# Kernel tuning notes

Measured on AMD Instinct MI355X. Metric: run time of the kernel, lower is better.

The kernel has to match this reference:

```python
import jax, jax.numpy as jnp
from jax import lax
import numpy as np

DN = ('NCH', 'OIH', 'NCH')

def conv1d(x, w, b, stride, pad):
    # x: (B,C,L), w: (O,I,K) torch Conv1d layout
    y = lax.conv_general_dilated(x, w, (stride,), [(pad, pad)], dimension_numbers=DN)
    return y + b[None, :, None]

def convt1d(x, w, b, stride, pad, out_pad):
    # w: (I,O,K) torch ConvTranspose1d layout -> flip + swap to (O,I,K)
    k = w.shape[-1]
    w2 = jnp.flip(w, -1).transpose(1, 0, 2)
    y = lax.conv_general_dilated(x, w2, (1,), [(k - 1 - pad, k - 1 - pad + out_pad)],
                                 lhs_dilation=(stride,), dimension_numbers=DN)
    return y + b[None, :, None]

def setup_inputs() -> dict:
    key = jax.random.key(0)
    ks = iter(jax.random.split(key, 32))
    def w_init(k, shape):
        fan_in = shape[1] * shape[2]
        return jax.random.normal(k, shape, jnp.float32) * (1.0 / np.sqrt(fan_in))
    inp = {}
    inp['waveform'] = jax.random.normal(next(ks), (8, 65536), jnp.float32)
    # encoder Conv1d weights (O,I,K)
    enc_shapes = [(64, 1, 15), (128, 64, 15), (256, 128, 15), (512, 256, 15), (512, 512, 7)]
    for i, s in enumerate(enc_shapes, 1):
        inp[f'e{i}w'] = w_init(next(ks), s)
        inp[f'e{i}b'] = jnp.zeros((s[0],), jnp.float32)
    # codebook, uniform(-1/K, 1/K) as in torch init
    K = 1024
    inp['codebook'] = jax.random.uniform(next(ks), (K, 512), jnp.float32, -1.0 / K, 1.0 / K)
    # decoder ConvTranspose1d weights (I,O,K)
    dec_shapes = [(512, 512, 7), (512, 256, 15), (256, 128, 15), (128, 64, 15), (64, 1, 15)]
    for i, s in enumerate(dec_shapes, 1):
        inp[f'd{i}w'] = w_init(next(ks), (s[1], s[0], s[2])).transpose(1, 0, 2)
        inp[f'd{i}b'] = jnp.zeros((s[1],), jnp.float32)
    return inp

def reference(waveform, e1w, e1b, e2w, e2b, e3w, e3b, e4w, e4b, e5w, e5b,
              codebook, d1w, d1b, d2w, d2b, d3w, d3b, d4w, d4b, d5w, d5b):
    elu = jax.nn.elu
    x = waveform[:, None, :]                       # (B,1,T)
    x = elu(conv1d(x, e1w, e1b, 1, 7))
    x = elu(conv1d(x, e2w, e2b, 2, 7))
    x = elu(conv1d(x, e3w, e3b, 2, 7))
    x = elu(conv1d(x, e4w, e4b, 2, 7))
    x = conv1d(x, e5w, e5b, 1, 3)                  # (B,D,T')
    emb = x.transpose(0, 2, 1)                     # (B,T',D)
    B, Tq, D = emb.shape
    flat = emb.reshape(-1, D)                      # (N,D)
    dists = (jnp.sum(flat * flat, axis=1, keepdims=True)
             + jnp.sum(codebook * codebook, axis=1)
             - 2.0 * flat @ codebook.T)            # (N,K)
    idx = jnp.argmin(dists, axis=1)                # (N,)
    q_flat = codebook[idx]                         # gather == one-hot matmul
    quantized = q_flat.reshape(B, Tq, D)
    commitment_loss = 0.25 * jnp.mean((lax.stop_gradient(quantized) - emb) ** 2)
    quantized_st = emb + lax.stop_gradient(quantized - emb)
    codes = idx.reshape(B, Tq)
    y = quantized_st.transpose(0, 2, 1)            # (B,D,T')
    y = elu(convt1d(y, d1w, d1b, 1, 3, 0))
    y = elu(convt1d(y, d2w, d2b, 2, 7, 1))
    y = elu(convt1d(y, d3w, d3b, 2, 7, 1))
    y = elu(convt1d(y, d4w, d4b, 2, 7, 1))
    y = jnp.tanh(convt1d(y, d5w, d5b, 1, 7, 0))    # (B,1,T)
    reconstructed = y[:, 0, :]                     # (B,T)
    recon_loss = jnp.mean(jnp.abs(reconstructed - waveform))
    return reconstructed, quantized_st, codes, commitment_loss, recon_loss
```

## Files before the change

kernel.cpp:

```cpp
#include <hip/hip_runtime.h>
#include <hip/hip_bf16.h>
#include <math.h>

#define DEV __device__ __forceinline__

typedef __attribute__((ext_vector_type(8))) short s16x8;
typedef __attribute__((ext_vector_type(4))) float f32x4;

DEV float elu_f(float v) { return v > 0.0f ? v : (float)expm1((double)v); }
DEV float elu_fast(float v) { return v > 0.0f ? v : expm1f(v); }

DEV unsigned short f2bf(float f) {
  unsigned u = __float_as_uint(f);
  return (unsigned short)((u + 0x7fffu + ((u >> 16) & 1u)) >> 16);
}
DEV float bf2f(unsigned short s) { return __uint_as_float(((unsigned)s) << 16); }

constexpr int ceil_div_c(int a, int b) { return (a > 0) ? (a + b - 1) / b : -((-a) / b); }

template<int K, int S, int PAD, int ACT>
__global__ __launch_bounds__(256) void conv1d_k(
    const float* __restrict__ x, const float* __restrict__ w,
    const float* __restrict__ bias, float* __restrict__ y,
    int Cin, int Cout, int Lin, int Lout)
{
  constexpr int PT = 8;
  constexpr int W  = (PT - 1) * S + K;
  constexpr int M0 = (4 - (PAD & 3)) & 3;
  constexpr int NQ = (M0 + W + 3) / 4;
  constexpr int CC = 16;
  constexpr int KP = (K + 3) & ~3;

  const int lane = threadIdx.x & 63;
  const int wv   = threadIdx.x >> 6;
  const int b    = blockIdx.z;
  const int cob  = blockIdx.y * 16;
  const int t0   = (blockIdx.x * 64 + lane) * PT;

  __shared__ __align__(16) float wl[16][CC][KP];

  float acc[4][PT];
  #pragma unroll
  for (int cc = 0; cc < 4; ++cc)
    #pragma unroll
    for (int g = 0; g < PT; ++g) acc[cc][g] = 0.0f;

  const float* xb  = x + (size_t)b * Cin * Lin;
  const int start = t0 * S - PAD;
  const int vbase = start - M0;
  const bool fast = (vbase >= 0) && (vbase + 4 * NQ <= Lin);

  for (int c0 = 0; c0 < Cin; c0 += CC) {
    const int cn = (Cin - c0 < CC) ? (Cin - c0) : CC;
    __syncthreads();
    for (int i = threadIdx.x; i < 16 * cn * K; i += 256) {
      int cc  = i / (cn * K);
      int rem = i - cc * (cn * K);
      int ci  = rem / K;
      int k   = rem - ci * K;
      wl[cc][ci][k] = w[((size_t)(cob + cc) * Cin + (c0 + ci)) * K + k];
    }
    __syncthreads();
    #pragma unroll 1
    for (int ci = 0; ci < cn; ++ci) {
      const float* xp = xb + (size_t)(c0 + ci) * Lin;
      float xr[W];
      if (fast) {
        float4 q[NQ];
        const float4* qp = (const float4*)(xp + vbase);
        #pragma unroll
        for (int j = 0; j < NQ; ++j) q[j] = qp[j];
        #pragma unroll
        for (int j = 0; j < W; ++j) xr[j] = ((const float*)q)[M0 + j];
      } else {
        #pragma unroll
        for (int j = 0; j < W; ++j) {
          int ix = start + j;
          xr[j] = (ix >= 0 && ix < Lin) ? xp[ix] : 0.0f;
        }
      }
      #pragma unroll
      for (int cc = 0; cc < 4; ++cc) {
        float wk[KP];
        const float4* wq = (const float4*)(&wl[wv * 4 + cc][ci][0]);
        #pragma unroll
        for (int q4 = 0; q4 < KP / 4; ++q4) {
          float4 t = wq[q4];
          wk[q4*4+0] = t.x; wk[q4*4+1] = t.y; wk[q4*4+2] = t.z; wk[q4*4+3] = t.w;
        }
        #pragma unroll
        for (int k = 0; k < K; ++k) {
          const float wv_ = wk[k];
          #pragma unroll
          for (int g = 0; g < PT; ++g)
            acc[cc][g] = fmaf(wv_, xr[g * S + k], acc[cc][g]);
        }
      }
    }
  }

  #pragma unroll
  for (int cc = 0; cc < 4; ++cc) {
    const int co = cob + wv * 4 + cc;
    const float bv = bias[co];
    float res[PT];
    #pragma unroll
    for (int g = 0; g < PT; ++g) {
      float v = acc[cc][g] + bv;
      if (ACT == 1) v = elu_f(v);
      res[g] = v;
    }
    float* yp = y + ((size_t)b * Cout + co) * Lout + t0;
    *(float4*)(yp)     = make_float4(res[0], res[1], res[2], res[3]);
    *(float4*)(yp + 4) = make_float4(res[4], res[5], res[6], res[7]);
  }
}

__global__ __launch_bounds__(256) void transpose_k(
    const float* __restrict__ in, float* __restrict__ out, int R, int S_)
{
  __shared__ float tile[32][33];
  const int b  = blockIdx.z;
  const int r0 = blockIdx.y * 32;
  const int s0 = blockIdx.x * 32;
  const float* ib = in + (size_t)b * R * S_;
  float* ob = out + (size_t)b * R * S_;
  const int tx = threadIdx.x, ty = threadIdx.y;
  #pragma unroll
  for (int i = 0; i < 32; i += 8)
    tile[ty + i][tx] = ib[(size_t)(r0 + ty + i) * S_ + s0 + tx];
  __syncthreads();
  #pragma unroll
  for (int i = 0; i < 32; i += 8)
    ob[(size_t)(s0 + ty + i) * R + r0 + tx] = tile[tx][ty + i];
}

DEV float np_sumsq_128(const float* a) {
  float r[8];
  #pragma unroll
  for (int j = 0; j < 8; ++j) r[j] = __fmul_rn(a[j], a[j]);
  #pragma unroll
  for (int i = 8; i < 128; i += 8) {
    #pragma unroll
    for (int j = 0; j < 8; ++j)
      r[j] = __fadd_rn(r[j], __fmul_rn(a[i + j], a[i + j]));
  }
  float s01 = __fadd_rn(r[0], r[1]), s23 = __fadd_rn(r[2], r[3]);
  float s45 = __fadd_rn(r[4], r[5]), s67 = __fadd_rn(r[6], r[7]);
  return __fadd_rn(__fadd_rn(s01, s23), __fadd_rn(s45, s67));
}
DEV float np_sumsq_512(const float* a) {
  float s0 = np_sumsq_128(a);
  float s1 = np_sumsq_128(a + 128);
  float s2 = np_sumsq_128(a + 256);
  float s3 = np_sumsq_128(a + 384);
  return __fadd_rn(__fadd_rn(s0, s1), __fadd_rn(s2, s3));
}

__global__ __launch_bounds__(256) void rowsumsq_k(
    const float* __restrict__ in, float* __restrict__ out, int nrows)
{
  const int r = blockIdx.x * 256 + threadIdx.x;
  if (r >= nrows) return;
  out[r] = np_sumsq_512(in + (size_t)r * 512);
}

__global__ __launch_bounds__(256) void vq_k(
    const float* __restrict__ embT, const float* __restrict__ cb,
    const float* __restrict__ t1, const float* __restrict__ cnorm,
    float* __restrict__ qout, float* __restrict__ codes, float* __restrict__ pc)
{
  __shared__ __align__(16) float xs[8][512];
  __shared__ float rv[4][8];
  __shared__ int   ri[4][8];
  __shared__ int   bidx[8];
  __shared__ float cred[4];

  const int tid  = threadIdx.x;
  const int row0 = blockIdx.x * 8;

  for (int i = tid * 4; i < 4096; i += 1024)
    *(float4*)((float*)xs + i) = *(const float4*)(embT + (size_t)row0 * 512 + i);
  __syncthreads();

  float acc[4][8];
  #pragma unroll
  for (int j = 0; j < 4; ++j)
    #pragma unroll
    for (int r = 0; r < 8; ++r) acc[j][r] = 0.0f;

  const float* cbp = cb + (size_t)tid * 512;
  #pragma unroll 1
  for (int d0 = 0; d0 < 512; d0 += 4) {
    float4 xv[8];
    #pragma unroll
    for (int r = 0; r < 8; ++r) xv[r] = *(const float4*)&xs[r][d0];
    #pragma unroll
    for (int j = 0; j < 4; ++j) {
      float4 cv = *(const float4*)(cbp + (size_t)j * 256 * 512 + d0);
      #pragma unroll
      for (int r = 0; r < 8; ++r) {
        acc[j][r] = fmaf(cv.x, xv[r].x, acc[j][r]);
        acc[j][r] = fmaf(cv.y, xv[r].y, acc[j][r]);
        acc[j][r] = fmaf(cv.z, xv[r].z, acc[j][r]);
        acc[j][r] = fmaf(cv.w, xv[r].w, acc[j][r]);
      }
    }
  }

  float cnj[4];
  #pragma unroll
  for (int j = 0; j < 4; ++j) cnj[j] = cnorm[tid + 256 * j];
  float t1r[8];
  #pragma unroll
  for (int r = 0; r < 8; ++r) t1r[r] = t1[row0 + r];

  const int lane = tid & 63, wv = tid >> 6;
  #pragma unroll 1
  for (int r = 0; r < 8; ++r) {
    float bv = 0.0f; int bi = 0;
    #pragma unroll
    for (int j = 0; j < 4; ++j) {
      float dv = __fsub_rn(__fadd_rn(t1r[r], cnj[j]), __fmul_rn(2.0f, acc[j][r]));
      int ki = tid + 256 * j;
      if (j == 0 || dv < bv || (dv == bv && ki < bi)) { bv = dv; bi = ki; }
    }
    #pragma unroll
    for (int off = 32; off; off >>= 1) {
      float ov = __shfl_xor(bv, off);
      int   oi = __shfl_xor(bi, off);
      if (ov < bv || (ov == bv && oi < bi)) { bv = ov; bi = oi; }
    }
    if (lane == 0) { rv[wv][r] = bv; ri[wv][r] = bi; }
  }
  __syncthreads();
  if (tid < 8) {
    float bv = rv[0][tid]; int bi = ri[0][tid];
    #pragma unroll
    for (int wq = 1; wq < 4; ++wq) {
      float ov = rv[wq][tid]; int oi = ri[wq][tid];
      if (ov < bv || (ov == bv && oi < bi)) { bv = ov; bi = oi; }
    }
    bidx[tid] = bi;
    codes[row0 + tid] = (float)bi;
  }
  __syncthreads();

  float csum = 0.0f;
  for (int i = tid * 4; i < 4096; i += 1024) {
    int r = i >> 9, d = i & 511;
    float4 qv = *(const float4*)(cb + (size_t)bidx[r] * 512 + d);
    *(float4*)(qout + (size_t)(row0 + r) * 512 + d) = qv;
    float dx = qv.x - xs[r][d],     dy = qv.y - xs[r][d + 1];
    float dz = qv.z - xs[r][d + 2], dw = qv.w - xs[r][d + 3];
    csum += dx * dx + dy * dy + dz * dz + dw * dw;
  }
  #pragma unroll
  for (int off = 32; off; off >>= 1) csum += __shfl_xor(csum, off);
  if (lane == 0) cred[wv] = csum;
  __syncthreads();
  if (tid == 0) pc[blockIdx.x] = cred[0] + cred[1] + cred[2] + cred[3];
}

__global__ __launch_bounds__(256) void f32_to_bf16_k(
    const float* __restrict__ in, unsigned short* __restrict__ out, int n4)
{
  int i = blockIdx.x * 256 + threadIdx.x;
  if (i >= n4) return;
  float4 v = *(const float4*)(in + (size_t)i * 4);
  ushort4 o;
  o.x = f2bf(v.x); o.y = f2bf(v.y); o.z = f2bf(v.z); o.w = f2bf(v.w);
  *(ushort4*)(out + (size_t)i * 4) = o;
}

__global__ __launch_bounds__(256) void zero_zbuf_k(unsigned short* z) {
  z[blockIdx.x * 256 + threadIdx.x] = 0;
}

__global__ __launch_bounds__(256) void prepack_w_k(
    const float* __restrict__ w, unsigned short* __restrict__ wp,
    int Cin, int Cout, int K, int T, int m0, int ms)
{
  int id = blockIdx.x * 256 + threadIdx.x;
  int tot = T * Cin * Cout;
  if (id >= tot) return;
  int jj  = id / (Cin * Cout);
  int rem = id - jj * (Cin * Cout);
  int ci  = rem / Cout;
  int co  = rem - ci * Cout;
  int m   = m0 + ms * jj;
  float v = w[((size_t)ci * Cout + co) * K + m];
  size_t dst = ((size_t)((jj * (Cin >> 5) + (ci >> 5)) * 4 + ((ci & 31) >> 3))) * ((size_t)Cout * 8)
             + (size_t)co * 8 + (ci & 7);
  wp[dst] = f2bf(v);
}

__global__ __launch_bounds__(256) void mfma_convt_k(
    const unsigned short* __restrict__ xb, const unsigned short* __restrict__ wp,
    const float* __restrict__ bias, unsigned short* __restrict__ yb,
    const unsigned short* __restrict__ zbuf,
    int Cin, int Cout, int Lin, int Lout, int S, int p, int T, int OFF0)
{
  const int lane = threadIdx.x & 63;
  const int wv   = threadIdx.x >> 6;
  const int r    = lane & 15;
  const int g    = lane >> 4;
  const int b    = blockIdx.z;
  const int u0   = blockIdx.x * 64 + wv * 16;
  const int co0  = blockIdx.y * 16;
  const int CB   = Cin >> 5;

  f32x4 acc = {0.f, 0.f, 0.f, 0.f};
  const unsigned short* xbb = xb + (size_t)b * Lin * Cin + g * 8;
  const unsigned short* zp  = zbuf + g * 8;
  const unsigned short* wpb = wp + (size_t)(co0 + r) * 8 + (size_t)g * Cout * 8;
  const size_t bstride = (size_t)4 * Cout * 8;

  const float bv = bias[co0 + r];

  #pragma unroll 1
  for (int jj = 0; jj < T; ++jj) {
    int u = u0 + r + OFF0 - jj;
    bool val = (u >= 0) && (u < Lin);
    const unsigned short* ap = val ? (xbb + (size_t)u * Cin) : zp;
    const unsigned short* bp = wpb + (size_t)jj * CB * bstride;
    #pragma unroll 2
    for (int cb = 0; cb < CB; ++cb) {
      s16x8 a  = *(const s16x8*)(ap + cb * 32);
      s16x8 bf = *(const s16x8*)(bp + (size_t)cb * bstride);
      acc = __builtin_amdgcn_mfma_f32_16x16x32_bf16(a, bf, acc, 0, 0, 0);
    }
  }

  #pragma unroll
  for (int reg = 0; reg < 4; ++reg) {
    int u  = u0 + g * 4 + reg;
    int o  = S * u + p;
    float v = elu_fast(acc[reg] + bv);
    yb[((size_t)b * Lout + o) * Cout + (co0 + r)] = f2bf(v);
  }
}

__global__ __launch_bounds__(256) void convt_final_bf16_k(
    const unsigned short* __restrict__ xb, const float* __restrict__ w,
    const float* __restrict__ bias, float* __restrict__ y)
{
  __shared__ float wl[64][16];
  for (int i = threadIdx.x; i < 64 * 15; i += 256) wl[i / 15][i % 15] = w[i];
  __syncthreads();
  const int b = blockIdx.y;
  const int o = blockIdx.x * 256 + threadIdx.x;
  float acc = 0.0f;
  #pragma unroll 1
  for (int m = 0; m < 15; ++m) {
    int i = o + 7 - m;
    if (i < 0 || i >= 65536) continue;
    const unsigned short* xp = xb + ((size_t)b * 65536 + i) * 64;
    #pragma unroll
    for (int c8 = 0; c8 < 8; ++c8) {
      s16x8 xv = *(const s16x8*)(xp + c8 * 8);
      #pragma unroll
      for (int k = 0; k < 8; ++k)
        acc = fmaf(wl[c8 * 8 + k][m], bf2f((unsigned short)xv[k]), acc);
    }
  }
  y[(size_t)b * 65536 + o] = tanhf(acc + bias[0]);
}

__global__ __launch_bounds__(256) void absdiff_part_k(
    const float* __restrict__ a, const float* __restrict__ b, float* __restrict__ pr)
{
  __shared__ float cred[4];
  const int tid  = threadIdx.x;
  const int base = blockIdx.x * 2048;
  float s = 0.0f;
  for (int i = tid * 4; i < 2048; i += 1024) {
    float4 x = *(const float4*)(a + base + i);
    float4 y = *(const float4*)(b + base + i);
    s += fabsf(x.x - y.x) + fabsf(x.y - y.y) + fabsf(x.z - y.z) + fabsf(x.w - y.w);
  }
  #pragma unroll
  for (int off = 32; off; off >>= 1) s += __shfl_xor(s, off);
  const int lane = tid & 63, wv = tid >> 6;
  if (lane == 0) cred[wv] = s;
  __syncthreads();
  if (tid == 0) pr[blockIdx.x] = cred[0] + cred[1] + cred[2] + cred[3];
}

__global__ __launch_bounds__(256) void finalize_k(
    const float* __restrict__ pc, const float* __restrict__ pr, float* __restrict__ outp)
{
  __shared__ float red[4];
  const int tid = threadIdx.x;
  const int lane = tid & 63, wv = tid >> 6;

  float s = 0.0f;
  for (int i = tid; i < 8192; i += 256) s += pc[i];
  #pragma unroll
  for (int off = 32; off; off >>= 1) s += __shfl_xor(s, off);
  if (lane == 0) red[wv] = s;
  __syncthreads();
  if (tid == 0) outp[0] = 0.25f * (red[0] + red[1] + red[2] + red[3]) / 33554432.0f;
  __syncthreads();

  float s2 = 0.0f;
  if (tid < 64) {
    for (int i = tid; i < 256; i += 64) s2 += pr[i];
    #pragma unroll
    for (int off = 32; off; off >>= 1) s2 += __shfl_xor(s2, off);
    if (tid == 0) outp[1] = s2 / 524288.0f;
  }
}

extern "C" void kernel_launch(void* const* d_in, const int* in_sizes, int n_in,
                              void* d_out, int out_size, void* d_ws, size_t ws_size,
                              hipStream_t stream) {
  const float* wave = (const float*)d_in[0];
  const float* e1w = (const float*)d_in[1];  const float* e1b = (const float*)d_in[2];
  const float* e2w = (const float*)d_in[3];  const float* e2b = (const float*)d_in[4];
  const float* e3w = (const float*)d_in[5];  const float* e3b = (const float*)d_in[6];
  const float* e4w = (const float*)d_in[7];  const float* e4b = (const float*)d_in[8];
  const float* e5w = (const float*)d_in[9];  const float* e5b = (const float*)d_in[10];
  const float* cb  = (const float*)d_in[11];
  const float* d1w = (const float*)d_in[12]; const float* d1b = (const float*)d_in[13];
  const float* d2w = (const float*)d_in[14]; const float* d2b = (const float*)d_in[15];
  const float* d3w = (const float*)d_in[16]; const float* d3b = (const float*)d_in[17];
  const float* d4w = (const float*)d_in[18]; const float* d4b = (const float*)d_in[19];
  const float* d5w = (const float*)d_in[20]; const float* d5b = (const float*)d_in[21];

  float* out = (float*)d_out;
  float* recon  = out;
  float* qout   = out + 524288;
  float* codes  = out + 34078720;
  float* losses = out + 34144256;

  float* A   = (float*)d_ws;
  float* Bb  = A + 33554432;
  float* t1  = Bb + 33554432;
  float* cn  = t1 + 65536;
  float* pc  = cn + 1024;
  float* pr  = pc + 8192;

  unsigned short* qb  = (unsigned short*)A;
  unsigned short* yb1 = (unsigned short*)Bb;
  unsigned short* yb2 = (unsigned short*)A;
  unsigned short* yb3 = (unsigned short*)(Bb + 16777216);
  unsigned short* yb4 = (unsigned short*)A;
  unsigned short* wsp   = (unsigned short*)(A + 16777216);
  unsigned short* zbuf  = wsp;
  unsigned short* wp1   = zbuf + 1024;
  unsigned short* wp2e  = wp1  + 1835008;
  unsigned short* wp2o  = wp2e + 917504;
  unsigned short* wp3e  = wp2o + 1048576;
  unsigned short* wp3o  = wp3e + 229376;
  unsigned short* wp4e  = wp3o + 262144;
  unsigned short* wp4o  = wp4e + 57344;

  dim3 blk(256);

  conv1d_k<15,1,7,1><<<dim3(128,  4, 8), blk, 0, stream>>>(wave, e1w, e1b, A,   1,  64, 65536, 65536);
  conv1d_k<15,2,7,1><<<dim3( 64,  8, 8), blk, 0, stream>>>(A,    e2w, e2b, Bb, 64, 128, 65536, 32768);
  conv1d_k<15,2,7,1><<<dim3( 32, 16, 8), blk, 0, stream>>>(Bb,   e3w, e3b, A, 128, 256, 32768, 16384);
  conv1d_k<15,2,7,1><<<dim3( 16, 32, 8), blk, 0, stream>>>(A,    e4w, e4b, Bb,256, 512, 16384,  8192);
  conv1d_k< 7,1,3,0><<<dim3( 16, 32, 8), blk, 0, stream>>>(Bb,   e5w, e5b, A, 512, 512,  8192,  8192);

  transpose_k<<<dim3(256, 16, 8), dim3(32, 8), 0, stream>>>(A, Bb, 512, 8192);
  rowsumsq_k<<<dim3(256), blk, 0, stream>>>(Bb, t1, 65536);
  rowsumsq_k<<<dim3(4),   blk, 0, stream>>>(cb, cn, 1024);
  vq_k<<<dim3(8192), blk, 0, stream>>>(Bb, cb, t1, cn, qout, codes, pc);

  f32_to_bf16_k<<<dim3(32768), blk, 0, stream>>>(qout, qb, 8388608);
  zero_zbuf_k<<<dim3(4), blk, 0, stream>>>(zbuf);
  prepack_w_k<<<dim3(7168), blk, 0, stream>>>(d1w, wp1, 512, 512, 7, 7, 0, 1);
  prepack_w_k<<<dim3(3584), blk, 0, stream>>>(d2w, wp2e, 512, 256, 15, 7, 1, 2);
  prepack_w_k<<<dim3(4096), blk, 0, stream>>>(d2w, wp2o, 512, 256, 15, 8, 0, 2);
  prepack_w_k<<<dim3( 896), blk, 0, stream>>>(d3w, wp3e, 256, 128, 15, 7, 1, 2);
  prepack_w_k<<<dim3(1024), blk, 0, stream>>>(d3w, wp3o, 256, 128, 15, 8, 0, 2);
  prepack_w_k<<<dim3( 224), blk, 0, stream>>>(d4w, wp4e, 128,  64, 15, 7, 1, 2);
  prepack_w_k<<<dim3( 256), blk, 0, stream>>>(d4w, wp4o, 128,  64, 15, 8, 0, 2);

  mfma_convt_k<<<dim3(128, 32, 8), blk, 0, stream>>>(qb,  wp1,  d1b, yb1, zbuf, 512, 512, 8192, 8192, 1, 0, 7, 3);
  mfma_convt_k<<<dim3(128, 16, 8), blk, 0, stream>>>(yb1, wp2e, d2b, yb2, zbuf, 512, 256, 8192, 16384, 2, 0, 7, 3);
  mfma_convt_k<<<dim3(128, 16, 8), blk, 0, stream>>>(yb1, wp2o, d2b, yb2, zbuf, 512, 256, 8192, 16384, 2, 1, 8, 4);
  mfma_convt_k<<<dim3(256,  8, 8), blk, 0, stream>>>(yb2, wp3e, d3b, yb3, zbuf, 256, 128, 16384, 32768, 2, 0, 7, 3);
  mfma_convt_k<<<dim3(256,  8, 8), blk, 0, stream>>>(yb2, wp3o, d3b, yb3, zbuf, 256, 128, 16384, 32768, 2, 1, 8, 4);
  mfma_convt_k<<<dim3(512,  4, 8), blk, 0, stream>>>(yb3, wp4e, d4b, yb4, zbuf, 128,  64, 32768, 65536, 2, 0, 7, 3);
  mfma_convt_k<<<dim3(512,  4, 8), blk, 0, stream>>>(yb3, wp4o, d4b, yb4, zbuf, 128,  64, 32768, 65536, 2, 1, 8, 4);
  convt_final_bf16_k<<<dim3(256, 8), blk, 0, stream>>>(yb4, d5w, d5b, recon);

  absdiff_part_k<<<dim3(256), blk, 0, stream>>>(recon, wave, pr);
  finalize_k<<<dim3(1), blk, 0, stream>>>(pc, pr, losses);
}
```

Before: 20.51 ms.

## Stage encoder conv input tiles in swizzled shared memory shared across waves

```diff
diff --git a/kernel.cpp b/kernel.cpp
--- a/kernel.cpp
+++ b/kernel.cpp
@@ -18,7 +18,7 @@
 
 constexpr int ceil_div_c(int a, int b) { return (a > 0) ? (a + b - 1) / b : -((-a) / b); }
 
-template<int K, int S, int PAD, int ACT>
+template<int K, int S, int PAD, int ACT, int CC>
 __global__ __launch_bounds__(256) void conv1d_k(
     const float* __restrict__ x, const float* __restrict__ w,
     const float* __restrict__ bias, float* __restrict__ y,
@@ -26,17 +26,18 @@
 {
   constexpr int PT = 8;
   constexpr int W  = (PT - 1) * S + K;
-  constexpr int M0 = (4 - (PAD & 3)) & 3;
-  constexpr int NQ = (M0 + W + 3) / 4;
-  constexpr int CC = 16;
+  constexpr int NR = (W + 3) / 4;
+  constexpr int RS = 63 * PT * S + NR * 4;
   constexpr int KP = (K + 3) & ~3;
 
   const int lane = threadIdx.x & 63;
   const int wv   = threadIdx.x >> 6;
   const int b    = blockIdx.z;
   const int cob  = blockIdx.y * 16;
-  const int t0   = (blockIdx.x * 64 + lane) * PT;
-
+  const int T0   = blockIdx.x * 512;
+  const int t0   = T0 + lane * PT;
+
+  __shared__ __align__(16) float xs[CC * RS];
   __shared__ __align__(16) float wl[16][CC][KP];
 
   float acc[4][PT];
@@ -45,14 +46,20 @@
     #pragma unroll
     for (int g = 0; g < PT; ++g) acc[cc][g] = 0.0f;
 
-  const float* xb  = x + (size_t)b * Cin * Lin;
-  const int start = t0 * S - PAD;
-  const int vbase = start - M0;
-  const bool fast = (vbase >= 0) && (vbase + 4 * NQ <= Lin);
+  const float* xb = x + (size_t)b * Cin * Lin;
+  const int G0 = T0 * S - PAD;
 
   for (int c0 = 0; c0 < Cin; c0 += CC) {
     const int cn = (Cin - c0 < CC) ? (Cin - c0) : CC;
     __syncthreads();
+    for (int i = threadIdx.x; i < cn * RS; i += 256) {
+      int r = i / RS, t = i - r * RS;
+      int gi = G0 + t;
+      float v = (gi >= 0 && gi < Lin) ? xb[(size_t)(c0 + r) * Lin + gi] : 0.0f;
+      int a = (r * RS + t) * 4;
+      a ^= ((a >> 7) & 3) << 4;
+      *(float*)((char*)xs + a) = v;
+    }
     for (int i = threadIdx.x; i < 16 * cn * K; i += 256) {
       int cc  = i / (cn * K);
       int rem = i - cc * (cn * K);
@@ -63,30 +70,23 @@
     __syncthreads();
     #pragma unroll 1
     for (int ci = 0; ci < cn; ++ci) {
-      const float* xp = xb + (size_t)(c0 + ci) * Lin;
-      float xr[W];
-      if (fast) {
-        float4 q[NQ];
-        const float4* qp = (const float4*)(xp + vbase);
-        #pragma unroll
-        for (int j = 0; j < NQ; ++j) q[j] = qp[j];
-        #pragma unroll
-        for (int j = 0; j < W; ++j) xr[j] = ((const float*)q)[M0 + j];
-      } else {
-        #pragma unroll
-        for (int j = 0; j < W; ++j) {
-          int ix = start + j;
-          xr[j] = (ix >= 0 && ix < Lin) ? xp[ix] : 0.0f;
-        }
+      float xr[4 * NR];
+      const int rb = ci * (RS * 4);
+      #pragma unroll
+      for (int jj = 0; jj < NR; ++jj) {
+        int a = rb + lane * (PT * S * 4) + jj * 16;
+        a ^= ((a >> 7) & 3) << 4;
+        float4 t = *(const float4*)((const char*)xs + a);
+        xr[4*jj+0] = t.x; xr[4*jj+1] = t.y; xr[4*jj+2] = t.z; xr[4*jj+3] = t.w;
       }
       #pragma unroll
       for (int cc = 0; cc < 4; ++cc) {
         float wk[KP];
-        const float4* wq = (const float4*)(&wl[wv * 4 + cc][ci][0]);
+        const float4* wq4 = (const float4*)(&wl[wv * 4 + cc][ci][0]);
         #pragma unroll
         for (int q4 = 0; q4 < KP / 4; ++q4) {
-          float4 t = wq[q4];
-          wk[q4*4+0] = t.x; wk[q4*4+1] = t.y; wk[q4*4+2] = t.z; wk[q4*4+3] = t.w;
+          float4 t = wq4[q4];
+          wk[4*q4+0] = t.x; wk[4*q4+1] = t.y; wk[4*q4+2] = t.z; wk[4*q4+3] = t.w;
         }
         #pragma unroll
         for (int k = 0; k < K; ++k) {
@@ -458,11 +458,11 @@
 
   dim3 blk(256);
 
-  conv1d_k<15,1,7,1><<<dim3(128,  4, 8), blk, 0, stream>>>(wave, e1w, e1b, A,   1,  64, 65536, 65536);
-  conv1d_k<15,2,7,1><<<dim3( 64,  8, 8), blk, 0, stream>>>(A,    e2w, e2b, Bb, 64, 128, 65536, 32768);
-  conv1d_k<15,2,7,1><<<dim3( 32, 16, 8), blk, 0, stream>>>(Bb,   e3w, e3b, A, 128, 256, 32768, 16384);
-  conv1d_k<15,2,7,1><<<dim3( 16, 32, 8), blk, 0, stream>>>(A,    e4w, e4b, Bb,256, 512, 16384,  8192);
-  conv1d_k< 7,1,3,0><<<dim3( 16, 32, 8), blk, 0, stream>>>(Bb,   e5w, e5b, A, 512, 512,  8192,  8192);
+  conv1d_k<15,1,7,1, 8><<<dim3(128,  4, 8), blk, 0, stream>>>(wave, e1w, e1b, A,   1,  64, 65536, 65536);
+  conv1d_k<15,2,7,1, 8><<<dim3( 64,  8, 8), blk, 0, stream>>>(A,    e2w, e2b, Bb, 64, 128, 65536, 32768);
+  conv1d_k<15,2,7,1, 8><<<dim3( 32, 16, 8), blk, 0, stream>>>(Bb,   e3w, e3b, A, 128, 256, 32768, 16384);
+  conv1d_k<15,2,7,1, 8><<<dim3( 16, 32, 8), blk, 0, stream>>>(A,    e4w, e4b, Bb,256, 512, 16384,  8192);
+  conv1d_k< 7,1,3,0,16><<<dim3( 16, 32, 8), blk, 0, stream>>>(Bb,   e5w, e5b, A, 512, 512,  8192,  8192);
 
   transpose_k<<<dim3(256, 16, 8), dim3(32, 8), 0, stream>>>(A, Bb, 512, 8192);
   rowsumsq_k<<<dim3(256), blk, 0, stream>>>(Bb, t1, 65536);
```

New measurement: 25.40 ms. +23.9%, slower.

## Replace LDS-staged encoder conv weights with scalar readfirstlane loads and specialized kernels

Applied to the files above, without the earlier changes.

```diff
diff --git a/kernel.cpp b/kernel.cpp
--- a/kernel.cpp
+++ b/kernel.cpp
@@ -16,96 +16,211 @@
 }
 DEV float bf2f(unsigned short s) { return __uint_as_float(((unsigned)s) << 16); }
 
-constexpr int ceil_div_c(int a, int b) { return (a > 0) ? (a + b - 1) / b : -((-a) / b); }
-
-template<int K, int S, int PAD, int ACT>
-__global__ __launch_bounds__(256) void conv1d_k(
+DEV float rfl(float v) {
+  return __uint_as_float(__builtin_amdgcn_readfirstlane(__float_as_uint(v)));
+}
+
+struct __attribute__((packed, aligned(4))) f4u { float x, y, z, w; };
+
+#define QC(Q, C) ((C) == 0 ? (Q).x : (C) == 1 ? (Q).y : (C) == 2 ? (Q).z : (Q).w)
+
+template<int ACT>
+__global__ __launch_bounds__(256) void conv1d_s2_k(
     const float* __restrict__ x, const float* __restrict__ w,
     const float* __restrict__ bias, float* __restrict__ y,
     int Cin, int Cout, int Lin, int Lout)
 {
-  constexpr int PT = 8;
-  constexpr int W  = (PT - 1) * S + K;
-  constexpr int M0 = (4 - (PAD & 3)) & 3;
-  constexpr int NQ = (M0 + W + 3) / 4;
-  constexpr int CC = 16;
-  constexpr int KP = (K + 3) & ~3;
-
   const int lane = threadIdx.x & 63;
   const int wv   = threadIdx.x >> 6;
   const int b    = blockIdx.z;
   const int cob  = blockIdx.y * 16;
-  const int t0   = (blockIdx.x * 64 + lane) * PT;
-
-  __shared__ __align__(16) float wl[16][CC][KP];
-
-  float acc[4][PT];
+  const int t0   = (blockIdx.x * 64 + lane) * 8;
+
+  float acc[4][8];
   #pragma unroll
   for (int cc = 0; cc < 4; ++cc)
     #pragma unroll
-    for (int g = 0; g < PT; ++g) acc[cc][g] = 0.0f;
-
-  const float* xb  = x + (size_t)b * Cin * Lin;
-  const int start = t0 * S - PAD;
-  const int vbase = start - M0;
-  const bool fast = (vbase >= 0) && (vbase + 4 * NQ <= Lin);
-
-  for (int c0 = 0; c0 < Cin; c0 += CC) {
-    const int cn = (Cin - c0 < CC) ? (Cin - c0) : CC;
-    __syncthreads();
-    for (int i = threadIdx.x; i < 16 * cn * K; i += 256) {
-      int cc  = i / (cn * K);
-      int rem = i - cc * (cn * K);
-      int ci  = rem / K;
-      int k   = rem - ci * K;
-      wl[cc][ci][k] = w[((size_t)(cob + cc) * Cin + (c0 + ci)) * K + k];
-    }
-    __syncthreads();
-    #pragma unroll 1
-    for (int ci = 0; ci < cn; ++ci) {
-      const float* xp = xb + (size_t)(c0 + ci) * Lin;
-      float xr[W];
-      if (fast) {
-        float4 q[NQ];
-        const float4* qp = (const float4*)(xp + vbase);
+    for (int g = 0; g < 8; ++g) acc[cc][g] = 0.0f;
+
+  const float* xb   = x + (size_t)b * Cin * Lin;
+  const int vbase  = t0 * 2 - 8;
+  const bool fast  = (vbase >= 0) && (vbase + 32 <= Lin);
+
+  const float* wr0 = w + (size_t)(cob + wv * 4 + 0) * Cin * 15;
+  const float* wr1 = w + (size_t)(cob + wv * 4 + 1) * Cin * 15;
+  const float* wr2 = w + (size_t)(cob + wv * 4 + 2) * Cin * 15;
+  const float* wr3 = w + (size_t)(cob + wv * 4 + 3) * Cin * 15;
+
+  float4 q0, q1, q2, q3, q4, q5, q6, q7;
+
+#define XV2(I) ((I) < 4 ? QC(q0,(I)&3) : (I) < 8 ? QC(q1,(I)&3) : (I) < 12 ? QC(q2,(I)&3) : \
+                (I) < 16 ? QC(q3,(I)&3) : (I) < 20 ? QC(q4,(I)&3) : (I) < 24 ? QC(q5,(I)&3) : \
+                (I) < 28 ? QC(q6,(I)&3) : QC(q7,(I)&3))
+#define LD4(Q, OFF)                                                           \
+  if (fast) { Q = *(const float4*)(xpB + vbase + (OFF)); }                    \
+  else {                                                                      \
+    int i0_ = vbase + (OFF);                                                  \
+    Q.x = (i0_ + 0 >= 0 && i0_ + 0 < Lin) ? xpB[i0_ + 0] : 0.0f;              \
+    Q.y = (i0_ + 1 >= 0 && i0_ + 1 < Lin) ? xpB[i0_ + 1] : 0.0f;              \
+    Q.z = (i0_ + 2 >= 0 && i0_ + 2 < Lin) ? xpB[i0_ + 2] : 0.0f;              \
+    Q.w = (i0_ + 3 >= 0 && i0_ + 3 < Lin) ? xpB[i0_ + 3] : 0.0f;              \
+  }
+
+  #pragma unroll 1
+  for (int ci = 0; ci < Cin; ++ci) {
+    const float* xpB = xb + (size_t)ci * Lin;
+    LD4(q0, 0)  LD4(q1, 4)  LD4(q2, 8)  LD4(q3, 12)  LD4(q4, 16)  LD4(q5, 20)
+
+    float wkf[4][15];
+    #pragma unroll
+    for (int cc = 0; cc < 4; ++cc) {
+      const float* wr = (cc == 0 ? wr0 : cc == 1 ? wr1 : cc == 2 ? wr2 : wr3)
+                        + (size_t)ci * 15;
+      f4u a = *(const f4u*)(wr);
+      f4u bq = *(const f4u*)(wr + 4);
+      f4u c = *(const f4u*)(wr + 8);
+      f4u d = *(const f4u*)(wr + 11);
+      wkf[cc][0]=rfl(a.x);  wkf[cc][1]=rfl(a.y);  wkf[cc][2]=rfl(a.z);  wkf[cc][3]=rfl(a.w);
+      wkf[cc][4]=rfl(bq.x); wkf[cc][5]=rfl(bq.y); wkf[cc][6]=rfl(bq.z); wkf[cc][7]=rfl(bq.w);
+      wkf[cc][8]=rfl(c.x);  wkf[cc][9]=rfl(c.y);  wkf[cc][10]=rfl(c.z);
+      wkf[cc][11]=rfl(d.x); wkf[cc][12]=rfl(d.y); wkf[cc][13]=rfl(d.z); wkf[cc][14]=rfl(d.w);
+    }
+
+    #pragma unroll
+    for (int cc = 0; cc < 4; ++cc)
+      #pragma unroll
+      for (int k = 0; k < 8; ++k) {
+        const float wv_ = wkf[cc][k];
         #pragma unroll
-        for (int j = 0; j < NQ; ++j) q[j] = qp[j];
+        for (int g = 0; g < 8; ++g)
+          acc[cc][g] = fmaf(wv_, XV2(1 + 2 * g + k), acc[cc][g]);
+      }
+
+    LD4(q6, 24)  LD4(q7, 28)
+
+    #pragma unroll
+    for (int cc = 0; cc < 4; ++cc)
+      #pragma unroll
+      for (int k = 8; k < 15; ++k) {
+        const float wv_ = wkf[cc][k];
         #pragma unroll
-        for (int j = 0; j < W; ++j) xr[j] = ((const float*)q)[M0 + j];
-      } else {
-        #pragma unroll
-        for (int j = 0; j < W; ++j) {
-          int ix = start + j;
-          xr[j] = (ix >= 0 && ix < Lin) ? xp[ix] : 0.0f;
-        }
+        for (int g = 0; g < 8; ++g)
+          acc[cc][g] = fmaf(wv_, XV2(1 + 2 * g + k), acc[cc][g]);
       }
-      #pragma unroll
-      for (int cc = 0; cc < 4; ++cc) {
-        float wk[KP];
-        const float4* wq = (const float4*)(&wl[wv * 4 + cc][ci][0]);
-        #pragma unroll
-        for (int q4 = 0; q4 < KP / 4; ++q4) {
-          float4 t = wq[q4];
-          wk[q4*4+0] = t.x; wk[q4*4+1] = t.y; wk[q4*4+2] = t.z; wk[q4*4+3] = t.w;
-        }
-        #pragma unroll
-        for (int k = 0; k < K; ++k) {
-          const float wv_ = wk[k];
-          #pragma unroll
-          for (int g = 0; g < PT; ++g)
-            acc[cc][g] = fmaf(wv_, xr[g * S + k], acc[cc][g]);
-        }
-      }
-    }
-  }
+  }
+#undef XV2
+#undef LD4
 
   #pragma unroll
   for (int cc = 0; cc < 4; ++cc) {
     const int co = cob + wv * 4 + cc;
     const float bv = bias[co];
-    float res[PT];
-    #pragma unroll
-    for (int g = 0; g < PT; ++g) {
+    float res[8];
+    #pragma unroll
+    for (int g = 0; g < 8; ++g) {
+      float v = acc[cc][g] + bv;
+      if (ACT == 1) v = elu_f(v);
+      res[g] = v;
+    }
+    float* yp = y + ((size_t)b * Cout + co) * Lout + t0;
+    *(float4*)(yp)     = make_float4(res[0], res[1], res[2], res[3]);
+    *(float4*)(yp + 4) = make_float4(res[4], res[5], res[6], res[7]);
+  }
+}
+
+template<int K, int PAD, int ACT>
+__global__ __launch_bounds__(256) void conv1d_s1_k(
+    const float* __restrict__ x, const float* __restrict__ w,
+    const float* __restrict__ bias, float* __restrict__ y,
+    int Cin, int Cout, int Lin, int Lout)
+{
+  constexpr int M0 = (4 - (PAD & 3)) & 3;
+  constexpr int W  = 7 + K;
+  constexpr int NQ = (M0 + W + 3) / 4;
+
+  const int lane = threadIdx.x & 63;
+  const int wv   = threadIdx.x >> 6;
+  const int b    = blockIdx.z;
+  const int cob  = blockIdx.y * 16;
+  const int t0   = (blockIdx.x * 64 + lane) * 8;
+
+  float acc[4][8];
+  #pragma unroll
+  for (int cc = 0; cc < 4; ++cc)
+    #pragma unroll
+    for (int g = 0; g < 8; ++g) acc[cc][g] = 0.0f;
+
+  const float* xb  = x + (size_t)b * Cin * Lin;
+  const int vbase = t0 - PAD - M0;
+  const bool fast = (vbase >= 0) && (vbase + 4 * NQ <= Lin);
+
+  const float* wr0 = w + (size_t)(cob + wv * 4 + 0) * Cin * K;
+  const float* wr1 = w + (size_t)(cob + wv * 4 + 1) * Cin * K;
+  const float* wr2 = w + (size_t)(cob + wv * 4 + 2) * Cin * K;
+  const float* wr3 = w + (size_t)(cob + wv * 4 + 3) * Cin * K;
+
+  float4 q0, q1, q2, q3, q4, q5;
+
+#define XV1(I) ((I) < 4 ? QC(q0,(I)&3) : (I) < 8 ? QC(q1,(I)&3) : (I) < 12 ? QC(q2,(I)&3) : \
+                (I) < 16 ? QC(q3,(I)&3) : (I) < 20 ? QC(q4,(I)&3) : QC(q5,(I)&3))
+#define LD4(Q, OFF)                                                           \
+  if (fast) { Q = *(const float4*)(xpB + vbase + (OFF)); }                    \
+  else {                                                                      \
+    int i0_ = vbase + (OFF);                                                  \
+    Q.x = (i0_ + 0 >= 0 && i0_ + 0 < Lin) ? xpB[i0_ + 0] : 0.0f;              \
+    Q.y = (i0_ + 1 >= 0 && i0_ + 1 < Lin) ? xpB[i0_ + 1] : 0.0f;              \
+    Q.z = (i0_ + 2 >= 0 && i0_ + 2 < Lin) ? xpB[i0_ + 2] : 0.0f;              \
+    Q.w = (i0_ + 3 >= 0 && i0_ + 3 < Lin) ? xpB[i0_ + 3] : 0.0f;              \
+  }
+
+  #pragma unroll 1
+  for (int ci = 0; ci < Cin; ++ci) {
+    const float* xpB = xb + (size_t)ci * Lin;
+    LD4(q0, 0)  LD4(q1, 4)  LD4(q2, 8)  LD4(q3, 12)
+    if constexpr (NQ > 4) { LD4(q4, 16) LD4(q5, 20) }
+
+    float wkf[4][K];
+    #pragma unroll
+    for (int cc = 0; cc < 4; ++cc) {
+      const float* wr = (cc == 0 ? wr0 : cc == 1 ? wr1 : cc == 2 ? wr2 : wr3)
+                        + (size_t)ci * K;
+      if constexpr (K == 15) {
+        f4u a = *(const f4u*)(wr);
+        f4u bq = *(const f4u*)(wr + 4);
+        f4u c = *(const f4u*)(wr + 8);
+        f4u d = *(const f4u*)(wr + 11);
+        wkf[cc][0]=rfl(a.x);  wkf[cc][1]=rfl(a.y);  wkf[cc][2]=rfl(a.z);  wkf[cc][3]=rfl(a.w);
+        wkf[cc][4]=rfl(bq.x); wkf[cc][5]=rfl(bq.y); wkf[cc][6]=rfl(bq.z); wkf[cc][7]=rfl(bq.w);
+        wkf[cc][8]=rfl(c.x);  wkf[cc][9]=rfl(c.y);  wkf[cc][10]=rfl(c.z);
+        wkf[cc][11]=rfl(d.x); wkf[cc][12]=rfl(d.y); wkf[cc][13]=rfl(d.z); wkf[cc][14]=rfl(d.w);
+      } else {
+        f4u a = *(const f4u*)(wr);
+        f4u bq = *(const f4u*)(wr + 3);
+        wkf[cc][0]=rfl(a.x); wkf[cc][1]=rfl(a.y); wkf[cc][2]=rfl(a.z); wkf[cc][3]=rfl(a.w);
+        wkf[cc][4]=rfl(bq.y); wkf[cc][5]=rfl(bq.z); wkf[cc][6]=rfl(bq.w);
+      }
+    }
+
+    #pragma unroll
+    for (int cc = 0; cc < 4; ++cc)
+      #pragma unroll
+      for (int k = 0; k < K; ++k) {
+        const float wv_ = wkf[cc][k];
+        #pragma unroll
+        for (int g = 0; g < 8; ++g)
+          acc[cc][g] = fmaf(wv_, XV1(M0 + g + k), acc[cc][g]);
+      }
+  }
+#undef XV1
+#undef LD4
+
+  #pragma unroll
+  for (int cc = 0; cc < 4; ++cc) {
+    const int co = cob + wv * 4 + cc;
+    const float bv = bias[co];
+    float res[8];
+    #pragma unroll
+    for (int g = 0; g < 8; ++g) {
       float v = acc[cc][g] + bv;
       if (ACT == 1) v = elu_f(v);
       res[g] = v;
@@ -458,11 +573,11 @@
 
   dim3 blk(256);
 
-  conv1d_k<15,1,7,1><<<dim3(128,  4, 8), blk, 0, stream>>>(wave, e1w, e1b, A,   1,  64, 65536, 65536);
-  conv1d_k<15,2,7,1><<<dim3( 64,  8, 8), blk, 0, stream>>>(A,    e2w, e2b, Bb, 64, 128, 65536, 32768);
-  conv1d_k<15,2,7,1><<<dim3( 32, 16, 8), blk, 0, stream>>>(Bb,   e3w, e3b, A, 128, 256, 32768, 16384);
-  conv1d_k<15,2,7,1><<<dim3( 16, 32, 8), blk, 0, stream>>>(A,    e4w, e4b, Bb,256, 512, 16384,  8192);
-  conv1d_k< 7,1,3,0><<<dim3( 16, 32, 8), blk, 0, stream>>>(Bb,   e5w, e5b, A, 512, 512,  8192,  8192);
+  conv1d_s1_k<15,7,1><<<dim3(128,  4, 8), blk, 0, stream>>>(wave, e1w, e1b, A,   1,  64, 65536, 65536);
+  conv1d_s2_k<1>     <<<dim3( 64,  8, 8), blk, 0, stream>>>(A,    e2w, e2b, Bb, 64, 128, 65536, 32768);
+  conv1d_s2_k<1>     <<<dim3( 32, 16, 8), blk, 0, stream>>>(Bb,   e3w, e3b, A, 128, 256, 32768, 16384);
+  conv1d_s2_k<1>     <<<dim3( 16, 32, 8), blk, 0, stream>>>(A,    e4w, e4b, Bb,256, 512, 16384,  8192);
+  conv1d_s1_k< 7,3,0><<<dim3( 16, 32, 8), blk, 0, stream>>>(Bb,   e5w, e5b, A, 512, 512,  8192,  8192);
 
   transpose_k<<<dim3(256, 16, 8), dim3(32, 8), 0, stream>>>(A, Bb, 512, 8192);
   rowsumsq_k<<<dim3(256), blk, 0, stream>>>(Bb, t1, 65536);
```

Result: slower. 24.25 ms (+18.2%).
